# Kernel optimization log

Measured on AMD Instinct MI355X. Metric: run time of the kernel, lower is better.

Reference implementation:

```python
import jax, jax.numpy as jnp
import numpy as np

B, SQ, SK, D = 8, 2048, 2048, 256

def setup_inputs() -> dict:
    key = jax.random.key(0)
    ks = jax.random.split(key, 8)
    x1 = jax.random.normal(ks[0], (B, SQ, D), dtype=jnp.float32)
    x2 = jax.random.normal(ks[1], (B, SK, D), dtype=jnp.float32)
    x3 = jax.random.normal(ks[2], (B, SK, D), dtype=jnp.float32)  # unused by the original forward (value=x3 is dead)
    mask = jax.random.bernoulli(ks[3], 0.8, (B, SK))
    scale = 0.02
    Wq = jax.random.normal(ks[4], (D, D), dtype=jnp.float32) * scale
    Wk = jax.random.normal(ks[5], (D, D), dtype=jnp.float32) * scale
    Wv = jax.random.normal(ks[6], (D, D), dtype=jnp.float32) * scale
    bq = jnp.zeros((D,), jnp.float32)
    bk = jnp.zeros((D,), jnp.float32)
    bv = jnp.zeros((D,), jnp.float32)
    return {"x1": x1, "x2": x2, "x3": x3, "Wq": Wq, "Wk": Wk, "Wv": Wv,
            "bq": bq, "bk": bk, "bv": bv, "mask": mask}

def reference(x1, x2, x3, Wq, Wk, Wv, bq, bk, bv, mask):
    d = x1.shape[-1]
    inv_sqrt_d = 1.0 / jnp.sqrt(jnp.asarray(d, x1.dtype))
    # Projections (single-head MHA with query scaling, as in torch MHA internals)
    q = (x1 @ Wq + bq) * inv_sqrt_d          # [B, SQ, D]
    k = x2 @ Wk + bk                          # [B, SK, D]
    v = x2 @ Wv + bv                          # forward_value(key): value projected from key input
    # Raw scores
    qk = jnp.einsum('bqd,bkd->bqk', q, k)     # [B, SQ, SK]
    # Mask-derived per-column rescale: qk /= (mask.size(0)/mask.sum(-2))**0.5
    m = mask.astype(qk.dtype)                 # [B, SK]
    col_count = jnp.sum(m, axis=0, keepdims=True)           # [1, SK]
    factor = jnp.sqrt(jnp.asarray(mask.shape[0], qk.dtype) / col_count)  # [1, SK]
    qk = qk / factor                          # broadcast over [B, SQ, SK]; div-by-inf -> 0 where column count is 0
    attn = jax.nn.softmax(qk, axis=-1)
    # dropout is identity in eval / p=0
    out = jnp.einsum('bqk,bkd->bqd', attn, v)  # [B, SQ, D]
    return out
```

## Files before the change

kernel.cpp:

```cpp
#include <hip/hip_runtime.h>
#include <hip/hip_bf16.h>
#include <math.h>

#define B_  8
#define SQ_ 2048
#define SK_ 2048
#define D_  256
#define NSPLIT 4
#define KEYS_PER_SPLIT (SK_ / NSPLIT)
#define NT (KEYS_PER_SPLIT / 32)

typedef __attribute__((ext_vector_type(8))) short bf16x8;
typedef __attribute__((ext_vector_type(4))) float f32x4;
typedef __attribute__((ext_vector_type(4))) unsigned short u16x4;
typedef __attribute__((ext_vector_type(8))) _Float16 f16x8;
typedef __attribute__((ext_vector_type(4))) _Float16 f16x4;
typedef __attribute__((ext_vector_type(4))) unsigned int u32x4;

static __device__ __forceinline__ unsigned short f2bf(float f) {
    unsigned int u = __builtin_bit_cast(unsigned int, f);
    u += 0x7FFFu + ((u >> 16) & 1u);
    return (unsigned short)(u >> 16);
}

static __device__ __forceinline__ void gld_lds16(const unsigned short* g, unsigned short* l) {
    __builtin_amdgcn_global_load_lds(
        (const __attribute__((address_space(1))) unsigned int*)g,
        (__attribute__((address_space(3))) unsigned int*)l, 16, 0, 0);
}

__global__ void prep_kernel(const float* __restrict__ Wq, const float* __restrict__ Wk,
                            const float* __restrict__ Wv, const int* __restrict__ mask,
                            unsigned short* __restrict__ wP, float* __restrict__ r) {
    int bid = blockIdx.x, tid = threadIdx.x;
    if (bid < 24) {
        int p = bid >> 3, c = bid & 7;
        const float* W = (p == 0 ? Wq : (p == 1 ? Wk : Wv));
#pragma unroll
        for (int it = 0; it < 4; it++) {
            int chunk = it * 256 + tid;
            int nt = chunk >> 6, lane = chunk & 63;
            int l15 = lane & 15, quad = lane >> 4;
            int n = nt * 16 + l15;
            unsigned short* dst = wP + (size_t)(((p * 8 + c) * 16 + nt) * 1024 + lane * 8);
#pragma unroll
            for (int j = 0; j < 8; j++)
                dst[j] = f2bf(W[(size_t)(c * 32 + quad * 8 + j) * D_ + n]);
        }
    } else {
        int s = (bid - 24) * 256 + tid;
        float c = 0.f;
#pragma unroll
        for (int b = 0; b < B_; b++) c += (mask[b * SK_ + s] != 0) ? 1.f : 0.f;
        r[s] = sqrtf(c * 0.125f);
    }
}

__global__ __launch_bounds__(256) void proj_kernel(
    const float* __restrict__ x1, const float* __restrict__ x2,
    const float* __restrict__ bq, const float* __restrict__ bk, const float* __restrict__ bv,
    const unsigned short* __restrict__ wP, const float* __restrict__ r,
    unsigned short* __restrict__ qb, unsigned short* __restrict__ kb,
    unsigned short* __restrict__ vt)
{
    __shared__ unsigned short sbuf[18432];
    const int tid = threadIdx.x;
    const int wv = tid >> 6, lane = tid & 63, l15 = lane & 15, quad = lane >> 4;
    const int mt = blockIdx.x, b = blockIdx.y, p = blockIdx.z;
    const int s0w = mt * 64 + wv * 16;

    const float* x = (p == 0 ? x1 : x2) + ((size_t)b * SQ_ + s0w + l15) * D_;
    const unsigned short* wbase = wP + (size_t)(p * 8) * 16 * 1024;
    const float* bias = (p == 0 ? bq : (p == 1 ? bk : bv));

    float4 xa[8], xb[8];
#pragma unroll
    for (int c = 0; c < 8; c++) {
        xa[c] = *(const float4*)(x + c * 32 + quad * 8);
        xb[c] = *(const float4*)(x + c * 32 + quad * 8 + 4);
    }
    bf16x8 af[8];
#pragma unroll
    for (int c = 0; c < 8; c++) {
        bf16x8 t;
        t[0] = (short)f2bf(xa[c].x); t[1] = (short)f2bf(xa[c].y);
        t[2] = (short)f2bf(xa[c].z); t[3] = (short)f2bf(xa[c].w);
        t[4] = (short)f2bf(xb[c].x); t[5] = (short)f2bf(xb[c].y);
        t[6] = (short)f2bf(xb[c].z); t[7] = (short)f2bf(xb[c].w);
        af[c] = t;
    }

    float bb[16];
#pragma unroll
    for (int nt = 0; nt < 16; nt++) bb[nt] = bias[nt * 16 + l15];

    f32x4 acc[16];
#pragma unroll
    for (int n = 0; n < 16; n++) acc[n] = (f32x4){0.f, 0.f, 0.f, 0.f};

#pragma unroll
    for (int c = 0; c < 8; c++) {
        const unsigned short* wc = wbase + (size_t)c * 16 * 1024 + lane * 8;
#pragma unroll
        for (int nt = 0; nt < 16; nt++) {
            bf16x8 wf = *(const bf16x8*)(wc + nt * 1024);
            acc[nt] = __builtin_amdgcn_mfma_f32_16x16x32_bf16(af[c], wf, acc[nt], 0, 0, 0);
        }
    }

    if (p == 2) {
#pragma unroll
        for (int nt = 0; nt < 16; nt++) {
            int d = nt * 16 + l15;
            u16x4 u;
#pragma unroll
            for (int g = 0; g < 4; g++) u[g] = f2bf(acc[nt][g] + bb[nt]);
            *(u16x4*)(sbuf + (size_t)d * 72 + wv * 16 + quad * 4) = u;
        }
        __syncthreads();
#pragma unroll
        for (int it = 0; it < 8; it++) {
            int chunk = it * 256 + tid;
            int d = chunk >> 3, s8 = chunk & 7;
            bf16x8 v = *(const bf16x8*)(sbuf + (size_t)d * 72 + s8 * 8);
            *(bf16x8*)(vt + ((size_t)b * D_ + d) * SK_ + mt * 64 + s8 * 8) = v;
        }
    } else {
        unsigned short* dst = (p == 0 ? qb : kb);
        float rv[4];
#pragma unroll
        for (int g = 0; g < 4; g++)
            rv[g] = (p == 1) ? r[s0w + quad * 4 + g] : 0.0625f;
        unsigned short* my = sbuf + wv * 2176;
#pragma unroll
        for (int h = 0; h < 2; h++) {
#pragma unroll
            for (int nt8 = 0; nt8 < 8; nt8++) {
                int nt = h * 8 + nt8;
#pragma unroll
                for (int g = 0; g < 4; g++) {
                    float v = (acc[nt][g] + bb[nt]) * rv[g];
                    my[(quad * 4 + g) * 136 + nt8 * 16 + l15] = f2bf(v);
                }
            }
            asm volatile("s_waitcnt lgkmcnt(0)" ::: "memory");
#pragma unroll
            for (int i2 = 0; i2 < 4; i2++) {
                int row = i2 * 4 + quad;
                bf16x8 v = *(const bf16x8*)(my + row * 136 + l15 * 8);
                *(bf16x8*)(dst + ((size_t)b * SQ_ + s0w + row) * D_ + h * 128 + l15 * 8) = v;
            }
        }
    }
}

__global__ __launch_bounds__(256, 2) void flash_kernel(
    const unsigned short* __restrict__ qb, const unsigned short* __restrict__ kb,
    const unsigned short* __restrict__ vt, _Float16* __restrict__ Op,
    float* __restrict__ lp)
{
    __shared__ unsigned short Ks[2][32 * 256];
    __shared__ unsigned short Vs[2][256 * 32];
    const int tid = threadIdx.x;
    const int wv = tid >> 6, lane = tid & 63, l15 = lane & 15, quad = lane >> 4;
    const int bid = blockIdx.x;
    const int g = bid & 31, q = bid >> 5;
    const int b = g >> 2, sp = g & 3;
    const int q0 = q * 128 + wv * 32;

    const unsigned short* kbb = kb + ((size_t)b * SK_ + sp * KEYS_PER_SPLIT) * D_;
    const unsigned short* vtb = vt + (size_t)b * D_ * SK_ + sp * KEYS_PER_SPLIT;

    int krow[4], kck[4], vd[4], vch[4];
#pragma unroll
    for (int i = 0; i < 4; i++) {
        int id = i * 256 + tid;
        krow[i] = id >> 5; kck[i] = (id & 31) ^ (krow[i] & 7);
        vd[i] = id >> 2;   vch[i] = (id & 3) ^ ((vd[i] >> 1) & 3);
    }

#pragma unroll
    for (int i = 0; i < 4; i++)
        gld_lds16(kbb + (size_t)krow[i] * D_ + kck[i] * 8, &Ks[0][(i * 256 + wv * 64) * 8]);
#pragma unroll
    for (int i = 0; i < 4; i++)
        gld_lds16(vtb + (size_t)vd[i] * SK_ + vch[i] * 8, &Vs[0][(i * 256 + wv * 64) * 8]);

    bf16x8 qf[2][8];
#pragma unroll
    for (int mt = 0; mt < 2; mt++) {
        const unsigned short* qrow = qb + ((size_t)(b * SQ_ + q0 + mt * 16 + l15)) * D_;
#pragma unroll
        for (int c = 0; c < 8; c++)
            qf[mt][c] = *(const bf16x8*)(qrow + c * 32 + quad * 8);
    }

    f32x4 o[2][16];
#pragma unroll
    for (int mt = 0; mt < 2; mt++)
#pragma unroll
        for (int n = 0; n < 16; n++) o[mt][n] = (f32x4){0.f, 0.f, 0.f, 0.f};
    float l_[2] = {0.f, 0.f};

    const int vsw = ((quad ^ ((l15 >> 1) & 3)) * 8);

    for (int kt = 0; kt < NT; kt++) {
        const int cur = kt & 1;
        __syncthreads();
        if (kt + 1 < NT) {
            const unsigned short* kn = kbb + (size_t)(kt + 1) * 32 * D_;
            const unsigned short* vn = vtb + (size_t)(kt + 1) * 32;
#pragma unroll
            for (int i = 0; i < 4; i++)
                gld_lds16(kn + (size_t)krow[i] * D_ + kck[i] * 8,
                          &Ks[cur ^ 1][(i * 256 + wv * 64) * 8]);
#pragma unroll
            for (int i = 0; i < 4; i++)
                gld_lds16(vn + (size_t)vd[i] * SK_ + vch[i] * 8,
                          &Vs[cur ^ 1][(i * 256 + wv * 64) * 8]);
        }

        f32x4 s[2][2];
        s[0][0] = (f32x4){0.f,0.f,0.f,0.f}; s[0][1] = (f32x4){0.f,0.f,0.f,0.f};
        s[1][0] = (f32x4){0.f,0.f,0.f,0.f}; s[1][1] = (f32x4){0.f,0.f,0.f,0.f};
        __builtin_amdgcn_s_setprio(1);
#pragma unroll
        for (int h = 0; h < 2; h++)
#pragma unroll
            for (int c = 0; c < 8; c++) {
                bf16x8 kf = *(const bf16x8*)(
                    &Ks[cur][(h * 16 + l15) * 256 + (((c * 4 + quad) ^ (l15 & 7)) * 8)]);
                s[0][h] = __builtin_amdgcn_mfma_f32_16x16x32_bf16(kf, qf[0][c], s[0][h], 0, 0, 0);
                s[1][h] = __builtin_amdgcn_mfma_f32_16x16x32_bf16(kf, qf[1][c], s[1][h], 0, 0, 0);
            }
        __builtin_amdgcn_s_setprio(0);

        bf16x8 pf[2];
#pragma unroll
        for (int mt = 0; mt < 2; mt++) {
            float e0 = __expf(s[mt][0][0]), e1 = __expf(s[mt][0][1]);
            float e2 = __expf(s[mt][0][2]), e3 = __expf(s[mt][0][3]);
            float f0 = __expf(s[mt][1][0]), f1 = __expf(s[mt][1][1]);
            float f2 = __expf(s[mt][1][2]), f3 = __expf(s[mt][1][3]);
            l_[mt] += (e0 + e1 + e2 + e3) + (f0 + f1 + f2 + f3);
            unsigned int pk0, pk1, pk2, pk3;
            asm("v_cvt_pk_bf16_f32 %0, %1, %2" : "=v"(pk0) : "v"(e0), "v"(e1));
            asm("v_cvt_pk_bf16_f32 %0, %1, %2" : "=v"(pk1) : "v"(e2), "v"(e3));
            asm("v_cvt_pk_bf16_f32 %0, %1, %2" : "=v"(pk2) : "v"(f0), "v"(f1));
            asm("v_cvt_pk_bf16_f32 %0, %1, %2" : "=v"(pk3) : "v"(f2), "v"(f3));
            asm("v_permlane32_swap_b32 %0, %1" : "+v"(pk0), "+v"(pk2));
            asm("v_permlane16_swap_b32 %0, %1" : "+v"(pk0), "+v"(pk2));
            asm("v_permlane32_swap_b32 %0, %1" : "+v"(pk1), "+v"(pk3));
            asm("v_permlane16_swap_b32 %0, %1" : "+v"(pk1), "+v"(pk3));
            u32x4 w = (u32x4){pk0, pk1, pk2, pk3};
            pf[mt] = __builtin_bit_cast(bf16x8, w);
        }

        __builtin_amdgcn_s_setprio(1);
#pragma unroll
        for (int n = 0; n < 16; n++) {
            bf16x8 vf = *(const bf16x8*)(&Vs[cur][(n * 16 + l15) * 32 + vsw]);
            o[0][n] = __builtin_amdgcn_mfma_f32_16x16x32_bf16(vf, pf[0], o[0][n], 0, 0, 0);
            o[1][n] = __builtin_amdgcn_mfma_f32_16x16x32_bf16(vf, pf[1], o[1][n], 0, 0, 0);
        }
        __builtin_amdgcn_s_setprio(0);
    }

#pragma unroll
    for (int mt = 0; mt < 2; mt++) {
        float t = l_[mt];
        t += __shfl_xor(t, 16, 64);
        t += __shfl_xor(t, 32, 64);
        l_[mt] = t;
    }

    _Float16* op = Op + ((size_t)(sp * B_ + b) * SQ_ + q0) * D_;
#pragma unroll
    for (int mt = 0; mt < 2; mt++) {
        _Float16* rowp = op + (size_t)(mt * 16 + l15) * D_ + quad * 4;
#pragma unroll
        for (int n = 0; n < 16; n++) {
            f16x4 v4;
#pragma unroll
            for (int g2 = 0; g2 < 4; g2++) v4[g2] = (_Float16)(o[mt][n][g2]);
            *(f16x4*)(rowp + n * 16) = v4;
        }
    }
    if (quad == 0) {
        float* lpp = lp + (size_t)(sp * B_ + b) * SQ_ + q0;
        lpp[l15] = l_[0];
        lpp[16 + l15] = l_[1];
    }
}

__global__ __launch_bounds__(256) void combine_kernel(
    const _Float16* __restrict__ Op, const float* __restrict__ lp,
    float* __restrict__ out)
{
    const int gid = blockIdx.x * 256 + threadIdx.x;
    const int row = gid >> 5;
    const size_t base = (size_t)gid * 8;
    float l = lp[row] + lp[B_ * SQ_ + row] + lp[2 * B_ * SQ_ + row] + lp[3 * B_ * SQ_ + row];
    float inv = 1.f / l;
    float acc[8] = {0,0,0,0,0,0,0,0};
#pragma unroll
    for (int sp = 0; sp < NSPLIT; sp++) {
        f16x8 v = *(const f16x8*)(Op + (size_t)sp * B_ * SQ_ * D_ + base);
#pragma unroll
        for (int j = 0; j < 8; j++) acc[j] += (float)v[j];
    }
    float4 r0 = {acc[0] * inv, acc[1] * inv, acc[2] * inv, acc[3] * inv};
    float4 r1 = {acc[4] * inv, acc[5] * inv, acc[6] * inv, acc[7] * inv};
    *(float4*)(out + base) = r0;
    *(float4*)(out + base + 4) = r1;
}

extern "C" void kernel_launch(void* const* d_in, const int* in_sizes, int n_in,
                              void* d_out, int out_size, void* d_ws, size_t ws_size,
                              hipStream_t stream)
{
    const float* x1 = (const float*)d_in[0];
    const float* x2 = (const float*)d_in[1];
    const float* Wq = (const float*)d_in[3];
    const float* Wk = (const float*)d_in[4];
    const float* Wv = (const float*)d_in[5];
    const float* bq = (const float*)d_in[6];
    const float* bk = (const float*)d_in[7];
    const float* bv = (const float*)d_in[8];
    const int*  mask = (const int*)d_in[9];
    float* out = (float*)d_out;

    char* ws = (char*)d_ws;
    unsigned short* qb = (unsigned short*)(ws);
    unsigned short* kb = (unsigned short*)(ws + 8388608);
    unsigned short* vt = (unsigned short*)(ws + 16777216);
    float*          r  = (float*)(ws + 25165824);
    float*          lp = (float*)(ws + 25174016);
    _Float16*       Op = (_Float16*)(ws + 25436160);
    unsigned short* wP = (unsigned short*)(ws + 25436160);

    prep_kernel<<<dim3(24 + SK_ / 256), 256, 0, stream>>>(Wq, Wk, Wv, mask, wP, r);
    proj_kernel<<<dim3(SQ_ / 64, B_, 3), 256, 0, stream>>>(x1, x2, bq, bk, bv, wP, r, qb, kb, vt);
    flash_kernel<<<dim3((SQ_ / 128) * B_ * NSPLIT), 256, 0, stream>>>(qb, kb, vt, Op, lp);
    combine_kernel<<<dim3((B_ * SQ_ * D_ / 8) / 256), 256, 0, stream>>>(Op, lp, out);
}
```

Baseline: 180.6 us.

## Pre-pack K/V into MFMA fragment layout and read directly from global

The projection kernel now writes K and V in a fragment-packed layout, so each lane's MFMA operand is one contiguous 16-byte chunk. The flash kernel drops its LDS double buffer, global_load_lds prefetches and per-tile __syncthreads, and loads K/V fragments straight from global/L2. Each of the four waves re-reads the same K/V tiles, relying on cache rather than shared memory. It also loses the explicit prefetch overlap. Launch bounds drop the min-2-blocks hint.

After: 281.8 us. +56.1%, slower.

```diff
diff --git a/kernel.cpp b/kernel.cpp
--- a/kernel.cpp
+++ b/kernel.cpp
@@ -23,12 +23,6 @@
     return (unsigned short)(u >> 16);
 }
 
-static __device__ __forceinline__ void gld_lds16(const unsigned short* g, unsigned short* l) {
-    __builtin_amdgcn_global_load_lds(
-        (const __attribute__((address_space(1))) unsigned int*)g,
-        (__attribute__((address_space(3))) unsigned int*)l, 16, 0, 0);
-}
-
 __global__ void prep_kernel(const float* __restrict__ Wq, const float* __restrict__ Wk,
                             const float* __restrict__ Wv, const int* __restrict__ mask,
                             unsigned short* __restrict__ wP, float* __restrict__ r) {
@@ -60,8 +54,8 @@
     const float* __restrict__ x1, const float* __restrict__ x2,
     const float* __restrict__ bq, const float* __restrict__ bk, const float* __restrict__ bv,
     const unsigned short* __restrict__ wP, const float* __restrict__ r,
-    unsigned short* __restrict__ qb, unsigned short* __restrict__ kb,
-    unsigned short* __restrict__ vt)
+    unsigned short* __restrict__ qb, unsigned short* __restrict__ kP,
+    unsigned short* __restrict__ vP)
 {
     __shared__ unsigned short sbuf[18432];
     const int tid = threadIdx.x;
@@ -121,22 +115,43 @@
 #pragma unroll
         for (int it = 0; it < 8; it++) {
             int chunk = it * 256 + tid;
-            int d = chunk >> 3, s8 = chunk & 7;
-            bf16x8 v = *(const bf16x8*)(sbuf + (size_t)d * 72 + s8 * 8);
-            *(bf16x8*)(vt + ((size_t)b * D_ + d) * SK_ + mt * 64 + s8 * 8) = v;
-        }
-    } else {
-        unsigned short* dst = (p == 0 ? qb : kb);
-        float rv[4];
-#pragma unroll
-        for (int g = 0; g < 4; g++)
-            rv[g] = (p == 1) ? r[s0w + quad * 4 + g] : 0.0625f;
+            int tt = chunk >> 10, n = (chunk >> 6) & 15, ln = chunk & 63;
+            bf16x8 v = *(const bf16x8*)(sbuf + (size_t)(n * 16 + (ln & 15)) * 72 + tt * 32 + (ln >> 4) * 8);
+            *(bf16x8*)(vP + (((size_t)(b * 64 + mt * 2 + tt) * 16 + n) * 512) + ln * 8) = v;
+        }
+    } else if (p == 0) {
+        float rv = 0.0625f;
         unsigned short* my = sbuf + wv * 2176;
 #pragma unroll
         for (int h = 0; h < 2; h++) {
 #pragma unroll
             for (int nt8 = 0; nt8 < 8; nt8++) {
                 int nt = h * 8 + nt8;
+#pragma unroll
+                for (int g = 0; g < 4; g++) {
+                    float v = (acc[nt][g] + bb[nt]) * rv;
+                    my[(quad * 4 + g) * 136 + nt8 * 16 + l15] = f2bf(v);
+                }
+            }
+            asm volatile("s_waitcnt lgkmcnt(0)" ::: "memory");
+#pragma unroll
+            for (int i2 = 0; i2 < 4; i2++) {
+                int row = i2 * 4 + quad;
+                bf16x8 v = *(const bf16x8*)(my + row * 136 + l15 * 8);
+                *(bf16x8*)(qb + ((size_t)(b * SQ_ + s0w + row)) * D_ + h * 128 + l15 * 8) = v;
+            }
+        }
+    } else {
+        const int t = mt * 2 + (wv >> 1), hfrag = wv & 1;
+        float rv[4];
+#pragma unroll
+        for (int g = 0; g < 4; g++) rv[g] = r[s0w + quad * 4 + g];
+        unsigned short* my = sbuf + wv * 2176;
+#pragma unroll
+        for (int hp = 0; hp < 2; hp++) {
+#pragma unroll
+            for (int nt8 = 0; nt8 < 8; nt8++) {
+                int nt = hp * 8 + nt8;
 #pragma unroll
                 for (int g = 0; g < 4; g++) {
                     float v = (acc[nt][g] + bb[nt]) * rv[g];
@@ -145,22 +160,19 @@
             }
             asm volatile("s_waitcnt lgkmcnt(0)" ::: "memory");
 #pragma unroll
-            for (int i2 = 0; i2 < 4; i2++) {
-                int row = i2 * 4 + quad;
-                bf16x8 v = *(const bf16x8*)(my + row * 136 + l15 * 8);
-                *(bf16x8*)(dst + ((size_t)b * SQ_ + s0w + row) * D_ + h * 128 + l15 * 8) = v;
-            }
-        }
-    }
-}
-
-__global__ __launch_bounds__(256, 2) void flash_kernel(
-    const unsigned short* __restrict__ qb, const unsigned short* __restrict__ kb,
-    const unsigned short* __restrict__ vt, _Float16* __restrict__ Op,
+            for (int cc = 0; cc < 4; cc++) {
+                bf16x8 v = *(const bf16x8*)(my + (size_t)l15 * 136 + cc * 32 + quad * 8);
+                *(bf16x8*)(kP + ((((size_t)(b * 64 + t) * 2 + hfrag) * 8 + hp * 4 + cc) * 512) + lane * 8) = v;
+            }
+        }
+    }
+}
+
+__global__ __launch_bounds__(256) void flash_kernel(
+    const unsigned short* __restrict__ qb, const unsigned short* __restrict__ kP,
+    const unsigned short* __restrict__ vP, _Float16* __restrict__ Op,
     float* __restrict__ lp)
 {
-    __shared__ unsigned short Ks[2][32 * 256];
-    __shared__ unsigned short Vs[2][256 * 32];
     const int tid = threadIdx.x;
     const int wv = tid >> 6, lane = tid & 63, l15 = lane & 15, quad = lane >> 4;
     const int bid = blockIdx.x;
@@ -168,23 +180,8 @@
     const int b = g >> 2, sp = g & 3;
     const int q0 = q * 128 + wv * 32;
 
-    const unsigned short* kbb = kb + ((size_t)b * SK_ + sp * KEYS_PER_SPLIT) * D_;
-    const unsigned short* vtb = vt + (size_t)b * D_ * SK_ + sp * KEYS_PER_SPLIT;
-
-    int krow[4], kck[4], vd[4], vch[4];
-#pragma unroll
-    for (int i = 0; i < 4; i++) {
-        int id = i * 256 + tid;
-        krow[i] = id >> 5; kck[i] = (id & 31) ^ (krow[i] & 7);
-        vd[i] = id >> 2;   vch[i] = (id & 3) ^ ((vd[i] >> 1) & 3);
-    }
-
-#pragma unroll
-    for (int i = 0; i < 4; i++)
-        gld_lds16(kbb + (size_t)krow[i] * D_ + kck[i] * 8, &Ks[0][(i * 256 + wv * 64) * 8]);
-#pragma unroll
-    for (int i = 0; i < 4; i++)
-        gld_lds16(vtb + (size_t)vd[i] * SK_ + vch[i] * 8, &Vs[0][(i * 256 + wv * 64) * 8]);
+    const unsigned short* kpb = kP + (size_t)(b * 64 + sp * 16) * 8192 + lane * 8;
+    const unsigned short* vpb = vP + (size_t)(b * 64 + sp * 16) * 8192 + lane * 8;
 
     bf16x8 qf[2][8];
 #pragma unroll
@@ -202,23 +199,9 @@
         for (int n = 0; n < 16; n++) o[mt][n] = (f32x4){0.f, 0.f, 0.f, 0.f};
     float l_[2] = {0.f, 0.f};
 
-    const int vsw = ((quad ^ ((l15 >> 1) & 3)) * 8);
-
     for (int kt = 0; kt < NT; kt++) {
-        const int cur = kt & 1;
-        __syncthreads();
-        if (kt + 1 < NT) {
-            const unsigned short* kn = kbb + (size_t)(kt + 1) * 32 * D_;
-            const unsigned short* vn = vtb + (size_t)(kt + 1) * 32;
-#pragma unroll
-            for (int i = 0; i < 4; i++)
-                gld_lds16(kn + (size_t)krow[i] * D_ + kck[i] * 8,
-                          &Ks[cur ^ 1][(i * 256 + wv * 64) * 8]);
-#pragma unroll
-            for (int i = 0; i < 4; i++)
-                gld_lds16(vn + (size_t)vd[i] * SK_ + vch[i] * 8,
-                          &Vs[cur ^ 1][(i * 256 + wv * 64) * 8]);
-        }
+        const unsigned short* kq = kpb + (size_t)kt * 8192;
+        const unsigned short* vq = vpb + (size_t)kt * 8192;
 
         f32x4 s[2][2];
         s[0][0] = (f32x4){0.f,0.f,0.f,0.f}; s[0][1] = (f32x4){0.f,0.f,0.f,0.f};
@@ -228,8 +211,7 @@
         for (int h = 0; h < 2; h++)
 #pragma unroll
             for (int c = 0; c < 8; c++) {
-                bf16x8 kf = *(const bf16x8*)(
-                    &Ks[cur][(h * 16 + l15) * 256 + (((c * 4 + quad) ^ (l15 & 7)) * 8)]);
+                bf16x8 kf = *(const bf16x8*)(kq + (h * 8 + c) * 512);
                 s[0][h] = __builtin_amdgcn_mfma_f32_16x16x32_bf16(kf, qf[0][c], s[0][h], 0, 0, 0);
                 s[1][h] = __builtin_amdgcn_mfma_f32_16x16x32_bf16(kf, qf[1][c], s[1][h], 0, 0, 0);
             }
@@ -259,7 +241,7 @@
         __builtin_amdgcn_s_setprio(1);
 #pragma unroll
         for (int n = 0; n < 16; n++) {
-            bf16x8 vf = *(const bf16x8*)(&Vs[cur][(n * 16 + l15) * 32 + vsw]);
+            bf16x8 vf = *(const bf16x8*)(vq + n * 512);
             o[0][n] = __builtin_amdgcn_mfma_f32_16x16x32_bf16(vf, pf[0], o[0][n], 0, 0, 0);
             o[1][n] = __builtin_amdgcn_mfma_f32_16x16x32_bf16(vf, pf[1], o[1][n], 0, 0, 0);
         }
@@ -332,15 +314,15 @@
 
     char* ws = (char*)d_ws;
     unsigned short* qb = (unsigned short*)(ws);
-    unsigned short* kb = (unsigned short*)(ws + 8388608);
-    unsigned short* vt = (unsigned short*)(ws + 16777216);
+    unsigned short* kP = (unsigned short*)(ws + 8388608);
+    unsigned short* vP = (unsigned short*)(ws + 16777216);
     float*          r  = (float*)(ws + 25165824);
     float*          lp = (float*)(ws + 25174016);
     _Float16*       Op = (_Float16*)(ws + 25436160);
     unsigned short* wP = (unsigned short*)(ws + 25436160);
 
     prep_kernel<<<dim3(24 + SK_ / 256), 256, 0, stream>>>(Wq, Wk, Wv, mask, wP, r);
-    proj_kernel<<<dim3(SQ_ / 64, B_, 3), 256, 0, stream>>>(x1, x2, bq, bk, bv, wP, r, qb, kb, vt);
-    flash_kernel<<<dim3((SQ_ / 128) * B_ * NSPLIT), 256, 0, stream>>>(qb, kb, vt, Op, lp);
+    proj_kernel<<<dim3(SQ_ / 64, B_, 3), 256, 0, stream>>>(x1, x2, bq, bk, bv, wP, r, qb, kP, vP);
+    flash_kernel<<<dim3((SQ_ / 128) * B_ * NSPLIT), 256, 0, stream>>>(qb, kP, vP, Op, lp);
     combine_kernel<<<dim3((B_ * SQ_ * D_ / 8) / 256), 256, 0, stream>>>(Op, lp, out);
 }
```
